# Kernel tuning notes

Measured on AMD Instinct MI355X. Metric: run time of the kernel, lower is better.

## Reference

```python
import jax, jax.numpy as jnp
import numpy as np
import math

N_H = 16

def _rope(x):
    # x: [b, h, n, d_k]; standard RoPE with half-split rotation
    n, d_k = x.shape[2], x.shape[3]
    inv_freq = 1.0 / (10000.0 ** (jnp.arange(0, d_k, 2, dtype=jnp.float32) / d_k))  # [d_k/2]
    freqs = jnp.arange(n, dtype=jnp.float32)[:, None] * inv_freq[None, :]            # [n, d_k/2]
    cos = jnp.concatenate([jnp.cos(freqs), jnp.cos(freqs)], axis=-1)[None, None]     # [1,1,n,d_k]
    sin = jnp.concatenate([jnp.sin(freqs), jnp.sin(freqs)], axis=-1)[None, None]
    x1, x2 = jnp.split(x, 2, axis=-1)
    rot = jnp.concatenate([-x2, x1], axis=-1)
    return x * cos + rot * sin


def setup_inputs() -> dict:
    key = jax.random.key(0)
    k1, k2, k3, k4 = jax.random.split(key, 4)
    b, n, d_m = 2, 1024, 2048
    x = jax.random.normal(k1, (b, n, d_m), dtype=jnp.float32)
    # causal mask (1 = keep, 0 = masked)
    m = jnp.tril(jnp.ones((n, n), dtype=jnp.int32))[None, None]  # [1,1,n,n]
    s = 1.0 / math.sqrt(d_m)
    Wqkv = jax.random.normal(k2, (d_m, 3 * d_m), dtype=jnp.float32) * s
    Wout = jax.random.normal(k3, (d_m, d_m), dtype=jnp.float32) * s
    bout = jax.random.normal(k4, (d_m,), dtype=jnp.float32) * 0.01
    return {"x": x, "m": m, "Wqkv": Wqkv, "Wout": Wout, "bout": bout}


def reference(x, m, Wqkv, Wout, bout):
    b, n, d = x.shape
    d_k = d // N_H
    qkv = (x @ Wqkv).reshape(b, n, 3, N_H, d_k)
    qkv = jnp.transpose(qkv, (2, 0, 3, 1, 4))  # [3, b, h, n, d_k]
    q, k, v = qkv[0], qkv[1], qkv[2]
    q, k = _rope(q), _rope(k)
    s = jnp.einsum('bhqd,bhkd->bhqk', q, k) / math.sqrt(d_k)
    s = jnp.where(m == 0, -jnp.inf, s)
    a = jax.nn.softmax(s, axis=-1)  # dropout is identity in eval / drop=0
    r = jnp.einsum('bhqk,bhkd->bhqd', a, v)
    r = jnp.transpose(r, (0, 2, 1, 3)).reshape(b, n, d)
    return r @ Wout + bout
```

## Files before the change

### kernel.cpp

```cpp
#include <hip/hip_runtime.h>
#include <math.h>

typedef unsigned short u16;
typedef unsigned int u32;
typedef __attribute__((ext_vector_type(8))) short short8;
typedef __attribute__((ext_vector_type(4))) float f32x4;

#define DEVI __device__ __forceinline__

DEVI u16 f2bf(float x) {
    union { float f; u32 u; } un; un.f = x;
    u32 u = un.u;
    return (u16)((u + 0x7fffu + ((u >> 16) & 1u)) >> 16);
}
DEVI float bf2f(u16 v) {
    union { u32 u; float f; } un; un.u = ((u32)v) << 16;
    return un.f;
}
DEVI f32x4 mfma_bf16(short8 a, short8 b, f32x4 c) {
    return __builtin_amdgcn_mfma_f32_16x16x32_bf16(a, b, c, 0, 0, 0);
}
DEVI void gload_lds16(const void* g, void* l) {
    __builtin_amdgcn_global_load_lds((const __attribute__((address_space(1))) u32*)g,
                                     (__attribute__((address_space(3))) u32*)l,
                                     16, 0, 0);
}

__global__ void k_prep(const float* __restrict__ x, const float* __restrict__ Wqkv,
                       const float* __restrict__ Wout, u16* __restrict__ x_bf,
                       u16* __restrict__ WqkvT, u16* __restrict__ WoutT) {
    __shared__ u16 tile[64][68];
    const int bid = blockIdx.x;
    if (bid < 4096) {
        long idx = ((long)bid * 256 + threadIdx.x) * 4;
        float4 v = *(const float4*)(x + idx);
        ushort4 o;
        o.x = f2bf(v.x); o.y = f2bf(v.y); o.z = f2bf(v.z); o.w = f2bf(v.w);
        *(ushort4*)(x_bf + idx) = o;
        return;
    }
    const float* in;
    u16* out;
    int R, C, bx, by;
    if (bid < 7168) {
        int lb = bid - 4096;
        in = Wqkv; out = WqkvT; R = 2048; C = 6144;
        bx = lb % 96; by = lb / 96;
    } else {
        int lb = bid - 7168;
        in = Wout; out = WoutT; R = 2048; C = 2048;
        bx = lb & 31; by = lb >> 5;
    }
    const int tx = threadIdx.x & 15, ty = threadIdx.x >> 4;
    const long r0 = (long)by * 64, c0 = (long)bx * 64;
#pragma unroll
    for (int p = 0; p < 4; ++p) {
        int r = ty + p * 16;
        float4 v = *(const float4*)(in + (r0 + r) * C + c0 + tx * 4);
        ushort4 o;
        o.x = f2bf(v.x); o.y = f2bf(v.y); o.z = f2bf(v.z); o.w = f2bf(v.w);
        *(ushort4*)&tile[r][tx * 4] = o;
    }
    __syncthreads();
#pragma unroll
    for (int p = 0; p < 4; ++p) {
        int rr = ty + p * 16;
        ushort4 o;
        o.x = tile[tx * 4 + 0][rr];
        o.y = tile[tx * 4 + 1][rr];
        o.z = tile[tx * 4 + 2][rr];
        o.w = tile[tx * 4 + 3][rr];
        *(ushort4*)(out + (c0 + rr) * R + r0 + tx * 4) = o;
    }
}

__global__ __launch_bounds__(512, 2) void k_qkv256(const u16* __restrict__ A,
                                                   const u16* __restrict__ BT,
                                                   u16* __restrict__ qb, u16* __restrict__ kb,
                                                   u16* __restrict__ vtb) {
    constexpr int K = 2048, NT = K / 64;
    __shared__ __align__(16) union SM {
        struct { u16 As[2][256 * 64]; u16 Bs[2][256 * 64]; } s;
        u16 T[128 * 264];
    } sm;
    const int tid = threadIdx.x;
    const int lane = tid & 63, wave = tid >> 6;
    const int lm = lane & 15, quad = lane >> 4;
    const int wm = wave >> 2, wn = wave & 3;
    const int bm = blockIdx.x, bn = blockIdx.y;
    const int srow = lane >> 3;
    const int scb = (lane & 7) ^ srow;
    const long arow0 = (long)bm * 256;
    const long brow0 = (long)bn * 256;

    f32x4 acc[8][4] = {};
    short8 a[8], b[4];

    auto stage = [&](const u16* __restrict__ src, long row0, u16* lds, int h, int kt) {
#pragma unroll
        for (int it = 0; it < 2; ++it) {
            int ch = wave * 2 + it;
            long r = h * 128 + ch * 8 + srow;
            gload_lds16(src + (row0 + r) * K + (long)kt * 64 + scb * 8,
                        (char*)lds + h * 16384 + ch * 1024);
        }
    };
    auto ldA = [&](int buf, int h) {
#pragma unroll
        for (int ii = 0; ii < 4; ++ii) {
            int row = h * 128 + wm * 64 + ii * 16 + lm;
#pragma unroll
            for (int ks = 0; ks < 2; ++ks) {
                int pc = (ks * 4 + quad) ^ (lm & 7);
                a[ii * 2 + ks] = *(const short8*)&sm.s.As[buf][row * 64 + pc * 8];
            }
        }
    };
    auto ldB = [&](int buf, int h) {
#pragma unroll
        for (int jj = 0; jj < 2; ++jj) {
            int row = h * 128 + wn * 32 + jj * 16 + lm;
#pragma unroll
            for (int ks = 0; ks < 2; ++ks) {
                int pc = (ks * 4 + quad) ^ (lm & 7);
                b[jj * 2 + ks] = *(const short8*)&sm.s.Bs[buf][row * 64 + pc * 8];
            }
        }
    };
    auto mmaq = [&](int ih, int jh) {
        __builtin_amdgcn_s_setprio(1);
#pragma unroll
        for (int ks = 0; ks < 2; ++ks)
#pragma unroll
            for (int ii = 0; ii < 4; ++ii)
#pragma unroll
                for (int jj = 0; jj < 2; ++jj)
                    acc[ih * 4 + ii][jh * 2 + jj] = mfma_bf16(
                        a[ii * 2 + ks], b[jj * 2 + ks], acc[ih * 4 + ii][jh * 2 + jj]);
        __builtin_amdgcn_s_setprio(0);
    };

#define VMW(n) asm volatile("s_waitcnt vmcnt(" #n ")" ::: "memory")
#define LGK0 asm volatile("s_waitcnt lgkmcnt(0)" ::: "memory")
#define BAR                            \
    do {                               \
        __builtin_amdgcn_s_barrier();  \
        asm volatile("" ::: "memory"); \
    } while (0)

    stage(A, arow0, sm.s.As[0], 0, 0);
    stage(BT, brow0, sm.s.Bs[0], 0, 0);
    stage(A, arow0, sm.s.As[0], 1, 0);
    stage(BT, brow0, sm.s.Bs[0], 1, 0);
    VMW(4);
    BAR;

    for (int t = 0; t < NT; ++t) {
        const int cur = t & 1, nxt = cur ^ 1;
        const int tn = (t + 1 < NT) ? t + 1 : t;
        ldA(cur, 0); ldB(cur, 0);
        stage(A, arow0, sm.s.As[nxt], 0, tn);
        BAR; LGK0;
        mmaq(0, 0);
        VMW(4);
        BAR;
        ldA(cur, 1);
        stage(BT, brow0, sm.s.Bs[nxt], 0, tn);
        BAR; LGK0;
        mmaq(1, 0);
        VMW(4);
        BAR;
        ldB(cur, 1);
        stage(A, arow0, sm.s.As[nxt], 1, tn);
        BAR; LGK0;
        mmaq(1, 1);
        BAR;
        ldA(cur, 0);
        stage(BT, brow0, sm.s.Bs[nxt], 1, tn);
        BAR; LGK0;
        mmaq(0, 1);
        VMW(4);
        BAR;
    }
    VMW(0);
    BAR;

    const int which = bn >> 3;
    const int hh = tid >> 8, t8 = tid & 255;
    const int h = (bn & 7) * 2 + hh;
#pragma unroll
    for (int rh = 0; rh < 2; ++rh) {
#pragma unroll
        for (int ii = 0; ii < 4; ++ii) {
            const int i = rh * 4 + ii;
            const int row_l = wm * 64 + ii * 16 + quad * 4;
#pragma unroll
            for (int j = 0; j < 4; ++j) {
                const int col_l = (j < 2 ? wn * 32 + j * 16 : 128 + wn * 32 + (j - 2) * 16) + lm;
#pragma unroll
                for (int r = 0; r < 4; ++r)
                    sm.T[(row_l + r) * 264 + col_l] = f2bf(acc[i][j][r]);
            }
        }
        __syncthreads();
        const int tb = bm * 256 + rh * 128;
        const int b_ = tb >> 10, p0 = tb & 1023;
        if (which < 2) {
            u16* dst = which ? kb : qb;
            const long hb = ((long)(b_ * 16 + h)) * 1024;
            const int i0 = (t8 * 4) & 63;
            const int pb = t8 >> 4;
            float inv[4];
#pragma unroll
            for (int e = 0; e < 4; ++e)
                inv[e] = exp2f(-(float)(i0 + e) * 0.20762050593045952f);
#pragma unroll
            for (int c = 0; c < 8; ++c) {
                const int pos_l = c * 16 + pb;
                ushort4 cu = *(const ushort4*)&sm.T[pos_l * 264 + hh * 128 + i0];
                ushort4 pa = *(const ushort4*)&sm.T[pos_l * 264 + hh * 128 + i0 + 64];
                const float pg = (float)(p0 + pos_l);
                ushort4 o1, o2;
                const u16* cp = (const u16*)&cu;
                const u16* pp = (const u16*)&pa;
                u16* o1p = (u16*)&o1;
                u16* o2p = (u16*)&o2;
#pragma unroll
                for (int e = 0; e < 4; ++e) {
                    float th = pg * inv[e];
                    float sv = __sinf(th), cv = __cosf(th);
                    float x1 = bf2f(cp[e]), x2 = bf2f(pp[e]);
                    o1p[e] = f2bf(x1 * cv - x2 * sv);
                    o2p[e] = f2bf(x2 * cv + x1 * sv);
                }
                const long rowb = (hb + p0 + pos_l) * 128;
                *(ushort4*)(dst + rowb + i0) = o1;
                *(ushort4*)(dst + rowb + i0 + 64) = o2;
            }
        } else {
            const long vrow = ((long)(b_ * 16 + h)) * 128;
#pragma unroll
            for (int c = 0; c < 8; ++c) {
                const int lin = c * 2048 + t8 * 8;
                const int dk = lin >> 7;
                const int ps = lin & 127;
                ushort4 o1, o2;
                u16* o1p = (u16*)&o1;
                u16* o2p = (u16*)&o2;
#pragma unroll
                for (int e = 0; e < 4; ++e) {
                    o1p[e] = sm.T[(ps + e) * 264 + hh * 128 + dk];
                    o2p[e] = sm.T[(ps + 4 + e) * 264 + hh * 128 + dk];
                }
                u16* dstv = vtb + (vrow + dk) * 1024 + p0 + ps;
                *(ushort4*)dstv = o1;
                *(ushort4*)(dstv + 4) = o2;
            }
        }
        if (rh == 0) __syncthreads();
    }
#undef VMW
#undef LGK0
#undef BAR
}

template <int EPI, int TM>
__global__ __launch_bounds__(256, 3) void k_gemm(const u16* __restrict__ A,
                                                 const u16* __restrict__ BT, int K,
                                                 u16* __restrict__ qb, u16* __restrict__ kb,
                                                 u16* __restrict__ vtb, float* __restrict__ out,
                                                 const float* __restrict__ bias) {
    constexpr int MI = TM / 32;
    constexpr int CA = TM / 32;
    __shared__ __align__(16) union SM {
        struct { u16 As[TM * 64]; u16 Bs[128 * 64]; } s;
        u16 T[EPI == 0 ? 128 * 132 : 8];
    } sm;
    const int tid = threadIdx.x;
    const int lane = tid & 63, wave = tid >> 6;
    const int lm = lane & 15, quad = lane >> 4;
    const int wm = wave >> 1, wn = wave & 1;
    const int bm = blockIdx.x, bn = blockIdx.y;

    f32x4 acc[MI][4] = {};

    const int srow = lane >> 3;
    const int scb = (lane & 7) ^ srow;
    const long arow0 = (long)bm * TM;
    const long brow0 = (long)bn * 128;

    for (int k0 = 0; k0 < K; k0 += 64) {
        __syncthreads();
#pragma unroll
        for (int it = 0; it < CA; ++it) {
            int ch = wave * CA + it;
            long r = ch * 8 + srow;
            gload_lds16(A + (arow0 + r) * K + k0 + scb * 8, (char*)sm.s.As + ch * 1024);
        }
#pragma unroll
        for (int it = 0; it < 4; ++it) {
            int ch = wave * 4 + it;
            long r = ch * 8 + srow;
            gload_lds16(BT + (brow0 + r) * K + k0 + scb * 8, (char*)sm.s.Bs + ch * 1024);
        }
        __syncthreads();
#pragma unroll
        for (int ko = 0; ko < 2; ++ko) {
            short8 af[MI], bf[4];
#pragma unroll
            for (int i = 0; i < MI; ++i) {
                int row = wm * (TM / 2) + i * 16 + lm;
                int pc = (ko * 4 + quad) ^ (lm & 7);
                af[i] = *(const short8*)&sm.s.As[row * 64 + pc * 8];
            }
#pragma unroll
            for (int j = 0; j < 4; ++j) {
                int row = wn * 64 + j * 16 + lm;
                int pc = (ko * 4 + quad) ^ (lm & 7);
                bf[j] = *(const short8*)&sm.s.Bs[row * 64 + pc * 8];
            }
#pragma unroll
            for (int i = 0; i < MI; ++i)
#pragma unroll
                for (int j = 0; j < 4; ++j)
                    acc[i][j] = mfma_bf16(af[i], bf[j], acc[i][j]);
        }
    }

    if constexpr (EPI == 1) {
        float bv[4];
#pragma unroll
        for (int j = 0; j < 4; ++j) bv[j] = bias[bn * 128 + wn * 64 + j * 16 + lm];
#pragma unroll
        for (int i = 0; i < MI; ++i) {
#pragma unroll
            for (int r = 0; r < 4; ++r) {
                const int row = bm * TM + wm * (TM / 2) + i * 16 + quad * 4 + r;
#pragma unroll
                for (int j = 0; j < 4; ++j) {
                    const int col = bn * 128 + wn * 64 + j * 16 + lm;
                    out[(long)row * 2048 + col] = acc[i][j][r] + bv[j];
                }
            }
        }
    }
}

__global__ __launch_bounds__(256, 3) void k_flash(const u16* __restrict__ Q,
                                                  const u16* __restrict__ Kb,
                                                  const u16* __restrict__ VT,
                                                  u16* __restrict__ R) {
    __shared__ u16 Ks[64 * 128];
    __shared__ u16 Vs[128 * 64];
    __shared__ u16 Ps[64 * 72];
    const int tid = threadIdx.x;
    const int lane = tid & 63, wave = tid >> 6;
    const int lm = lane & 15, quad = lane >> 4;
    const int id = blockIdx.x;
    const int g = id >> 8, rem = id & 255;
    const int bh = rem >> 3, s = rem & 7;
    const int qt = g ? (15 - s) : s;
    const long qkbase = (long)bh * 1024 * 128;
    const long vtbase = (long)bh * 128 * 1024;
    const int q0 = qt * 64;

    short8 qf[4];
    {
        const u16* qrow = Q + qkbase + (long)(q0 + wave * 16 + lm) * 128 + quad * 8;
#pragma unroll
        for (int kc = 0; kc < 4; ++kc) qf[kc] = *(const short8*)(qrow + kc * 32);
    }

    f32x4 o_acc[8] = {};
    float m_i = -INFINITY, l_i = 0.f;
    const float cl2e = 0.08838834764831845f * 1.4426950408889634f;

    const int kr = lane >> 4;
    const int vr = lane >> 3;
    const int vcb = (lane & 7) ^ vr;

    for (int kt = 0; kt <= qt; ++kt) {
        __syncthreads();
        {
#pragma unroll
            for (int it = 0; it < 4; ++it) {
                int ch = wave * 4 + it;
                int krow = ch * 4 + kr;
                int kchunk = (lane & 15) ^ (krow & 15);
                gload_lds16(Kb + qkbase + (long)(kt * 64 + krow) * 128 + kchunk * 8,
                            (char*)Ks + ch * 1024);
                int vrow = ch * 8 + vr;
                gload_lds16(VT + vtbase + (long)vrow * 1024 + kt * 64 + vcb * 8,
                            (char*)Vs + ch * 1024);
            }
        }
        __syncthreads();

        f32x4 s_acc[4] = {};
#pragma unroll
        for (int kc = 0; kc < 4; ++kc) {
#pragma unroll
            for (int mi = 0; mi < 4; ++mi) {
                int row = mi * 16 + lm;
                int pc = (kc * 4 + quad) ^ lm;
                short8 ak = *(const short8*)&Ks[row * 128 + pc * 8];
                s_acc[mi] = mfma_bf16(ak, qf[kc], s_acc[mi]);
            }
        }
        const int qg = q0 + wave * 16 + lm;
        float t[4][4];
        float cmax = -INFINITY;
#pragma unroll
        for (int mi = 0; mi < 4; ++mi)
#pragma unroll
            for (int r = 0; r < 4; ++r) {
                int kg = kt * 64 + mi * 16 + quad * 4 + r;
                float val = (kg <= qg) ? s_acc[mi][r] * cl2e : -INFINITY;
                t[mi][r] = val;
                cmax = fmaxf(cmax, val);
            }
        cmax = fmaxf(cmax, __shfl_xor(cmax, 16));
        cmax = fmaxf(cmax, __shfl_xor(cmax, 32));
        float m_new = fmaxf(m_i, cmax);
        float alpha = exp2f(m_i - m_new);
        float csum = 0.f;
#pragma unroll
        for (int mi = 0; mi < 4; ++mi)
#pragma unroll
            for (int r = 0; r < 4; ++r) {
                float p = exp2f(t[mi][r] - m_new);
                t[mi][r] = p;
                csum += p;
            }
        csum += __shfl_xor(csum, 16);
        csum += __shfl_xor(csum, 32);
        l_i = l_i * alpha + csum;
        m_i = m_new;
#pragma unroll
        for (int mi = 0; mi < 4; ++mi) {
            ushort4 pk;
            pk.x = f2bf(t[mi][0]); pk.y = f2bf(t[mi][1]);
            pk.z = f2bf(t[mi][2]); pk.w = f2bf(t[mi][3]);
            *(ushort4*)&Ps[(wave * 16 + lm) * 72 + mi * 16 + quad * 4] = pk;
        }
        float aq[4];
#pragma unroll
        for (int r = 0; r < 4; ++r) aq[r] = __shfl(alpha, quad * 4 + r, 64);
#pragma unroll
        for (int nt = 0; nt < 8; ++nt)
#pragma unroll
            for (int r = 0; r < 4; ++r) o_acc[nt][r] *= aq[r];
#pragma unroll
        for (int kc = 0; kc < 2; ++kc) {
            short8 ap = *(const short8*)&Ps[(wave * 16 + lm) * 72 + kc * 32 + quad * 8];
#pragma unroll
            for (int nt = 0; nt < 8; ++nt) {
                int row = nt * 16 + lm;
                int pc = (kc * 4 + quad) ^ (lm & 7);
                short8 bv = *(const short8*)&Vs[row * 64 + pc * 8];
                o_acc[nt] = mfma_bf16(ap, bv, o_acc[nt]);
            }
        }
    }
    float lq[4];
#pragma unroll
    for (int r = 0; r < 4; ++r) lq[r] = __shfl(l_i, quad * 4 + r, 64);
    const int b = bh >> 4, h = bh & 15;
#pragma unroll
    for (int nt = 0; nt < 8; ++nt)
#pragma unroll
        for (int r = 0; r < 4; ++r) {
            const int pos = q0 + wave * 16 + quad * 4 + r;
            const int col = h * 128 + nt * 16 + lm;
            R[((long)b * 1024 + pos) * 2048 + col] = f2bf(o_acc[nt][r] / lq[r]);
        }
}

extern "C" void kernel_launch(void* const* d_in, const int* in_sizes, int n_in,
                              void* d_out, int out_size, void* d_ws, size_t ws_size,
                              hipStream_t stream) {
    const float* x    = (const float*)d_in[0];
    const float* Wqkv = (const float*)d_in[2];
    const float* Wout = (const float*)d_in[3];
    const float* bout = (const float*)d_in[4];
    float* out = (float*)d_out;

    char* ws = (char*)d_ws;
    u16* x_bf  = (u16*)(ws);
    u16* rbuf  = x_bf;
    u16* WqkvT = (u16*)(ws + (8L << 20));
    u16* WoutT = (u16*)(ws + (32L << 20));
    u16* qbuf  = (u16*)(ws + (40L << 20));
    u16* kbuf  = (u16*)(ws + (48L << 20));
    u16* vtbuf = (u16*)(ws + (56L << 20));

    k_prep<<<8192, 256, 0, stream>>>(x, Wqkv, Wout, x_bf, WqkvT, WoutT);
    k_qkv256<<<dim3(8, 24), 512, 0, stream>>>(x_bf, WqkvT, qbuf, kbuf, vtbuf);
    k_flash<<<512, 256, 0, stream>>>(qbuf, kbuf, vtbuf, rbuf);
    k_gemm<1, 64><<<dim3(32, 16), 256, 0, stream>>>(rbuf, WoutT, 2048, nullptr, nullptr,
                                                    nullptr, out, bout);
}
```

Measured before the change: 255.4 us.

## Deepen GEMM prefetch so B halves and A upper half load two tiles ahead

Reworks the QKV GEMM's double-buffered global-to-LDS schedule. Each quarter-tile slot is now refilled for tile t+2 as soon as it has been read into registers, instead of waiting a whole tile. Most intermediate vmcnt waits are removed and a single wait per iteration allows up to six loads in flight. This is meant to hide more global memory latency behind the MFMA work, but it relies on the barrier ordering to keep the in-place slot reuse safe.

```diff
diff --git a/kernel.cpp b/kernel.cpp
--- a/kernel.cpp
+++ b/kernel.cpp
@@ -96,13 +96,22 @@
     f32x4 acc[8][4] = {};
     short8 a[8], b[4];
 
-    auto stage = [&](const u16* __restrict__ src, long row0, u16* lds, int h, int kt) {
+    auto stageA = [&](int buf, int h, int kt) {
 #pragma unroll
         for (int it = 0; it < 2; ++it) {
             int ch = wave * 2 + it;
             long r = h * 128 + ch * 8 + srow;
-            gload_lds16(src + (row0 + r) * K + (long)kt * 64 + scb * 8,
-                        (char*)lds + h * 16384 + ch * 1024);
+            gload_lds16(A + (arow0 + r) * K + (long)kt * 64 + scb * 8,
+                        (char*)&sm.s.As[buf][h * 8192] + ch * 1024);
+        }
+    };
+    auto stageB = [&](int buf, int h, int kt) {
+#pragma unroll
+        for (int it = 0; it < 2; ++it) {
+            int ch = wave * 2 + it;
+            long r = h * 128 + ch * 8 + srow;
+            gload_lds16(BT + (brow0 + r) * K + (long)kt * 64 + scb * 8,
+                        (char*)&sm.s.Bs[buf][h * 8192] + ch * 1024);
         }
     };
     auto ldA = [&](int buf, int h) {
@@ -148,38 +157,36 @@
         asm volatile("" ::: "memory"); \
     } while (0)
 
-    stage(A, arow0, sm.s.As[0], 0, 0);
-    stage(BT, brow0, sm.s.Bs[0], 0, 0);
-    stage(A, arow0, sm.s.As[0], 1, 0);
-    stage(BT, brow0, sm.s.Bs[0], 1, 0);
+    stageA(0, 0, 0); stageB(0, 0, 0); stageA(0, 1, 0); stageB(0, 1, 0);
     VMW(4);
+    stageB(1, 0, 1); stageA(1, 1, 1); stageB(1, 1, 1);
+    VMW(6);
     BAR;
 
     for (int t = 0; t < NT; ++t) {
         const int cur = t & 1, nxt = cur ^ 1;
-        const int tn = (t + 1 < NT) ? t + 1 : t;
+        const int t1 = (t + 1 < NT) ? t + 1 : NT - 1;
+        const int t2 = (t + 2 < NT) ? t + 2 : NT - 1;
         ldA(cur, 0); ldB(cur, 0);
-        stage(A, arow0, sm.s.As[nxt], 0, tn);
+        stageA(nxt, 0, t1);
         BAR; LGK0;
         mmaq(0, 0);
-        VMW(4);
         BAR;
         ldA(cur, 1);
-        stage(BT, brow0, sm.s.Bs[nxt], 0, tn);
+        stageB(cur, 0, t2);
         BAR; LGK0;
         mmaq(1, 0);
-        VMW(4);
         BAR;
         ldB(cur, 1);
-        stage(A, arow0, sm.s.As[nxt], 1, tn);
+        stageA(cur, 1, t2);
         BAR; LGK0;
         mmaq(1, 1);
         BAR;
         ldA(cur, 0);
-        stage(BT, brow0, sm.s.Bs[nxt], 1, tn);
+        stageB(cur, 1, t2);
         BAR; LGK0;
         mmaq(0, 1);
-        VMW(4);
+        VMW(6);
         BAR;
     }
     VMW(0);
```

Result: no change. 258.3 us (+1.2%).
